# Kernel tuning notes

Hardware: AMD Instinct MI355X
Metric: run time of the kernel (lower is better)

The kernel has to match this reference:

```python
import jax, jax.numpy as jnp
import numpy as np
from jax import lax

BN_EPS = 1e-5
PAD = ((2, 3), (1, 2))  # 'same' padding for kernel (6,4): H pad 5 -> (2,3), W pad 3 -> (1,2)
DN = ('NCHW', 'OIHW', 'NCHW')


def _conv_block(x, w, b, g, bt, m, v, pool):
    # pool(bn(relu(conv(pad(x))))) as in the torch module (eval-mode BN)
    x = lax.conv_general_dilated(x, w, (1, 1), PAD, dimension_numbers=DN)
    x = jax.nn.relu(x + b[None, :, None, None])
    scale = g / jnp.sqrt(v + BN_EPS)
    x = (x - m[None, :, None, None]) * scale[None, :, None, None] + bt[None, :, None, None]
    win = (1, 1) + pool
    return lax.reduce_window(x, -jnp.inf, lax.max, win, win, 'VALID')


def _fc_bn(x, w, b, g, bt, m, v):
    x = jax.nn.relu(x @ w.T + b)
    return (x - m) * (g / jnp.sqrt(v + BN_EPS)) + bt


def _apply_cnn(x, p):
    x = x[:, None, :, :]  # [N,1,72,64]
    x = _conv_block(x, p['conv1_w'], p['conv1_b'], p['bnc1_g'], p['bnc1_b'], p['bnc1_m'], p['bnc1_v'], (2, 2))
    x = _conv_block(x, p['conv2_w'], p['conv2_b'], p['bnc2_g'], p['bnc2_b'], p['bnc2_m'], p['bnc2_v'], (2, 2))
    x = _conv_block(x, p['conv3_w'], p['conv3_b'], p['bnc3_g'], p['bnc3_b'], p['bnc3_m'], p['bnc3_v'], (3, 4))
    x = x.reshape(x.shape[0], 6 * 4 * 64)  # NCHW contiguous flatten matches torch .view
    x = _fc_bn(x, p['fc1_w'], p['fc1_b'], p['bnf1_g'], p['bnf1_b'], p['bnf1_m'], p['bnf1_v'])
    x = _fc_bn(x, p['fc2_w'], p['fc2_b'], p['bnf2_g'], p['bnf2_b'], p['bnf2_m'], p['bnf2_v'])
    x = _fc_bn(x, p['fc3_w'], p['fc3_b'], p['bnf3_g'], p['bnf3_b'], p['bnf3_m'], p['bnf3_v'])
    # F.normalize(x, p=2, dim=1) with eps=1e-12
    nrm = jnp.linalg.norm(x, axis=1, keepdims=True)
    return x / jnp.maximum(nrm, 1e-12)


def _ssm(embeds):
    # pairwise L2 distances via Gram trick (replaces the O(n^2) python loop)
    sq = jnp.sum(embeds * embeds, axis=1)  # [n]
    d2 = sq[:, None] + sq[None, :] - 2.0 * (embeds @ embeds.T)
    dist = jnp.sqrt(jnp.maximum(d2, 1e-12))
    dist = jnp.where(d2 > 0, dist, 0.0)  # exact zeros on diagonal, nan-safe grad
    return dist / jnp.max(dist)


def setup_inputs() -> dict:
    key = jax.random.key(0)
    ks = iter(jax.random.split(key, 64))
    d = {'x': jax.random.normal(next(ks), (512, 72, 64), jnp.float32)}

    def nrm(shape, s=0.05):
        return jax.random.normal(next(ks), shape, jnp.float32) * s

    def add_bn(name, c):
        d[name + '_g'] = 1.0 + nrm((c,))
        d[name + '_b'] = nrm((c,))
        d[name + '_m'] = nrm((c,), 0.1)
        d[name + '_v'] = 0.5 + jax.random.uniform(next(ks), (c,), jnp.float32)

    d['conv1_w'] = nrm((16, 1, 6, 4), 0.2);  d['conv1_b'] = nrm((16,));  add_bn('bnc1', 16)
    d['conv2_w'] = nrm((32, 16, 6, 4), 0.1); d['conv2_b'] = nrm((32,));  add_bn('bnc2', 32)
    d['conv3_w'] = nrm((64, 32, 6, 4), 0.05); d['conv3_b'] = nrm((64,)); add_bn('bnc3', 64)
    d['fc1_w'] = nrm((512, 1536), 0.03); d['fc1_b'] = nrm((512,)); add_bn('bnf1', 512)
    d['fc2_w'] = nrm((256, 512), 0.05);  d['fc2_b'] = nrm((256,)); add_bn('bnf2', 256)
    d['fc3_w'] = nrm((128, 256), 0.07);  d['fc3_b'] = nrm((128,)); add_bn('bnf3', 128)
    return d


def reference(x,
              conv1_w, conv1_b, bnc1_g, bnc1_b, bnc1_m, bnc1_v,
              conv2_w, conv2_b, bnc2_g, bnc2_b, bnc2_m, bnc2_v,
              conv3_w, conv3_b, bnc3_g, bnc3_b, bnc3_m, bnc3_v,
              fc1_w, fc1_b, bnf1_g, bnf1_b, bnf1_m, bnf1_v,
              fc2_w, fc2_b, bnf2_g, bnf2_b, bnf2_m, bnf2_v,
              fc3_w, fc3_b, bnf3_g, bnf3_b, bnf3_m, bnf3_v):
    p = dict(conv1_w=conv1_w, conv1_b=conv1_b, bnc1_g=bnc1_g, bnc1_b=bnc1_b, bnc1_m=bnc1_m, bnc1_v=bnc1_v,
             conv2_w=conv2_w, conv2_b=conv2_b, bnc2_g=bnc2_g, bnc2_b=bnc2_b, bnc2_m=bnc2_m, bnc2_v=bnc2_v,
             conv3_w=conv3_w, conv3_b=conv3_b, bnc3_g=bnc3_g, bnc3_b=bnc3_b, bnc3_m=bnc3_m, bnc3_v=bnc3_v,
             fc1_w=fc1_w, fc1_b=fc1_b, bnf1_g=bnf1_g, bnf1_b=bnf1_b, bnf1_m=bnf1_m, bnf1_v=bnf1_v,
             fc2_w=fc2_w, fc2_b=fc2_b, bnf2_g=bnf2_g, bnf2_b=bnf2_b, bnf2_m=bnf2_m, bnf2_v=bnf2_v,
             fc3_w=fc3_w, fc3_b=fc3_b, bnf3_g=bnf3_g, bnf3_b=bnf3_b, bnf3_m=bnf3_m, bnf3_v=bnf3_v)
    embeds = _apply_cnn(x, p)  # [n, 128], L2-normalized
    return _ssm(embeds)        # [n, n]
```

## Files before the change

kernel.cpp:

```cpp
#include <hip/hip_runtime.h>
#include <math.h>


#define BN_EPS 1e-5f

typedef __attribute__((ext_vector_type(8))) short short8;
typedef __attribute__((ext_vector_type(4))) float f32x4;

__device__ __forceinline__ unsigned short f2bf(float f) {
    unsigned u = __float_as_uint(f);
    u += 0x7fffu + ((u >> 16) & 1u);
    return (unsigned short)(u >> 16);
}

__global__ __launch_bounds__(256) void repack_k(
    const float* __restrict__ w1, const float* __restrict__ w2,
    const float* __restrict__ w3,
    const float* __restrict__ fw1, const float* __restrict__ fw2,
    const float* __restrict__ fw3,
    unsigned short* __restrict__ wT1b,
    unsigned short* __restrict__ wT2b, unsigned short* __restrict__ wT3b,
    unsigned short* __restrict__ fw1b, unsigned short* __restrict__ fw2b,
    unsigned short* __restrict__ fw3b, unsigned* __restrict__ mxslot)
{
    int t = blockIdx.x * 256 + threadIdx.x;
    if (t == 0) *mxslot = 0u;
    if (t < 512) {
        int k = t & 31, oc = t >> 5;
        wT1b[t] = (k < 24) ? f2bf(w1[oc * 24 + k]) : (unsigned short)0;
    }
    if (t < 12288) {
        int k = t & 31, oc = (t >> 5) & 31, kk = t >> 10;
        int ky = kk >> 1, kxp = kk & 1;
        int hi = k >> 4, ic = k & 15;
        int kx = 2 * kxp + hi;
        wT2b[t] = f2bf(w2[((oc * 16 + ic) * 6 + ky) * 4 + kx]);
    }
    if (t < 49152) {
        int ic = t & 31, oc = (t >> 5) & 63, kk = t >> 11;
        int ky = kk >> 2, kx = kk & 3;
        wT3b[t] = f2bf(w3[((oc * 32 + ic) * 6 + ky) * 4 + kx]);
    }
    if (t < 786432) fw1b[t] = f2bf(fw1[t]);
    if (t < 131072) fw2b[t] = f2bf(fw2[t]);
    if (t < 32768)  fw3b[t] = f2bf(fw3[t]);
}

__global__ __launch_bounds__(512) void conv_all(
    const float* __restrict__ x, const unsigned short* __restrict__ wT1,
    const unsigned short* __restrict__ wT2, const unsigned short* __restrict__ wT3,
    const float* __restrict__ c1b, const float* __restrict__ g1,
    const float* __restrict__ b1, const float* __restrict__ m1,
    const float* __restrict__ v1,
    const float* __restrict__ c2b, const float* __restrict__ g2,
    const float* __restrict__ b2, const float* __restrict__ m2,
    const float* __restrict__ v2,
    const float* __restrict__ c3b, const float* __restrict__ g3,
    const float* __restrict__ b3, const float* __restrict__ m3,
    const float* __restrict__ v3,
    unsigned short* __restrict__ out3)
{
    __shared__ __align__(16) unsigned short s_out1[2 * 1476 * 8];
    __shared__ __align__(16) unsigned short s_un[4 * 480 * 8];
    const int tid = threadIdx.x, nl = blockIdx.x;
    const int lane = tid & 63, wave = tid >> 6;
    const int n = lane & 15, q = lane >> 4;
    unsigned short* pa = s_un;
    unsigned short* pb = s_un + 5534;

    {
        unsigned* z32 = (unsigned*)s_un;
        for (int i = tid; i < 5532; i += 512) z32[i] = 0u;
        uint4 z4; z4.x = z4.y = z4.z = z4.w = 0u;
        for (int pc = tid; pc < 324; pc += 512) {
            int row, colc;
            if (pc < 180) { row = pc / 36; colc = pc % 36; if (row >= 2) row += 36; }
            else { int pz = pc - 180; row = 2 + (pz >> 2); colc = (pz & 3) ? 32 + (pz & 3) : 0; }
            int cc = row * 36 + colc;
            *(uint4*)(s_out1 + cc * 8) = z4;
            *(uint4*)(s_out1 + 11808 + cc * 8) = z4;
        }
    }
    __syncthreads();
    {
        const float4* src = (const float4*)(x + (size_t)nl * 4608);
        for (int i = tid; i < 1152; i += 512) {
            float4 val = src[i];
            int f = i * 4, row = (f >> 6) + 2, c = (f & 63) + 1;
            unsigned short h0 = f2bf(val.x), h1 = f2bf(val.y);
            unsigned short h2 = f2bf(val.z), h3 = f2bf(val.w);
            unsigned short* ap = pa + row * 70 + c;
            ap[0] = h0; ap[1] = h1; ap[2] = h2; ap[3] = h3;
            unsigned* bp = (unsigned*)(pb + row * 70 + c + 1);
            bp[0] = (unsigned)h0 | ((unsigned)h1 << 16);
            bp[1] = (unsigned)h2 | ((unsigned)h3 << 16);
        }
    }
    const float sc1 = g1[n] * rsqrtf(v1[n] + BN_EPS);
    const float bb1 = c1b[n];
    const float mm1 = b1[n] - m1[n] * sc1;
    const short8 bfr1 = *(const short8*)(wT1 + n * 32 + q * 8);
    __syncthreads();

    for (int i = 0; i < 36; ++i) {
        int t = wave * 36 + i;
        int pooled = 4 * t + (n >> 2);
        int ph = pooled >> 5, pw = pooled & 31;
        int py = (n >> 1) & 1, px = n & 1;
        int oh = 2 * ph + py, ow = 2 * pw + px;
        int r0 = (oh + 2 * q) * 70;
        const unsigned* base = px ? (const unsigned*)(pb + r0 + ow + 1)
                                  : (const unsigned*)(pa + r0 + ow);
        uint4 uu;
        uu.x = base[0];  uu.y = base[1];
        uu.z = base[35]; uu.w = base[36];
        short8 afr = *reinterpret_cast<short8*>(&uu);
        f32x4 acc = (f32x4){0.f, 0.f, 0.f, 0.f};
        acc = __builtin_amdgcn_mfma_f32_16x16x32_bf16(afr, bfr1, acc, 0, 0, 0);
        int po = 4 * t + q, oph = po >> 5, opw = po & 31;
        float mx = fmaxf(fmaxf(acc[0], acc[1]), fmaxf(acc[2], acc[3]));
        float val = fmaxf(mx + bb1, 0.f) * sc1 + mm1;
        int cc = (oph + 2) * 36 + (opw + 1);
        s_out1[(n >> 3) * 11808 + cc * 8 + (n & 7)] = f2bf(val);
    }
    __syncthreads();
    {
        uint4 z4; z4.x = z4.y = z4.z = z4.w = 0u;
        for (int pc = tid; pc < 192; pc += 512) {
            int row, colc;
            if (pc < 120) { row = pc / 20; colc = pc % 20; if (row >= 2) row += 18; }
            else { int pz = pc - 120; row = 2 + (pz >> 2); colc = (pz & 3) ? 16 + (pz & 3) : 0; }
            int cc = row * 20 + colc;
            *(uint4*)(s_un + cc * 8) = z4;
            *(uint4*)(s_un + 3840 + cc * 8) = z4;
            *(uint4*)(s_un + 7680 + cc * 8) = z4;
            *(uint4*)(s_un + 11520 + cc * 8) = z4;
        }
    }
    float bnb2[2], bns2[2], bnm2[2];
#pragma unroll
    for (int nt = 0; nt < 2; ++nt) {
        int oc = nt * 16 + n;
        float sc = g2[oc] * rsqrtf(v2[oc] + BN_EPS);
        bnb2[nt] = c2b[oc]; bns2[nt] = sc; bnm2[nt] = b2[oc] - m2[oc] * sc;
    }
    __syncthreads();

    for (int pp = wave; pp < 36; pp += 8) {
        int ph = pp >> 1, half = pp & 1;
        const unsigned short* bB = s_out1 + (q & 1) * 11808 + (q >> 1) * 8
                                   + (half * 16 + n) * 8 + (2 * ph) * 288;
        f32x4 acc[2][2];
#pragma unroll
        for (int ab = 0; ab < 2; ++ab)
#pragma unroll
            for (int nt = 0; nt < 2; ++nt) acc[ab][nt] = (f32x4){0.f, 0.f, 0.f, 0.f};
#pragma unroll
        for (int ky = 0; ky < 6; ++ky)
#pragma unroll
            for (int kxp = 0; kxp < 2; ++kxp) {
                int kk = ky * 2 + kxp;
                short8 w0 = *(const short8*)(wT2 + ((size_t)(kk * 32 + n) * 32) + q * 8);
                short8 w1 = *(const short8*)(wT2 + ((size_t)(kk * 32 + 16 + n) * 32) + q * 8);
#pragma unroll
                for (int ab = 0; ab < 2; ++ab) {
                    short8 afr = *(const short8*)(bB + ((ab + ky) * 288 + kxp * 16));
                    acc[ab][0] = __builtin_amdgcn_mfma_f32_16x16x32_bf16(afr, w0, acc[ab][0], 0, 0, 0);
                    acc[ab][1] = __builtin_amdgcn_mfma_f32_16x16x32_bf16(afr, w1, acc[ab][1], 0, 0, 0);
                }
            }
        int pw0 = half * 8 + q * 2;
#pragma unroll
        for (int nt = 0; nt < 2; ++nt) {
            int oc = nt * 16 + n;
            float p0 = fmaxf(fmaxf(acc[0][nt][0], acc[0][nt][1]),
                             fmaxf(acc[1][nt][0], acc[1][nt][1]));
            float p1 = fmaxf(fmaxf(acc[0][nt][2], acc[0][nt][3]),
                             fmaxf(acc[1][nt][2], acc[1][nt][3]));
            p0 = fmaxf(p0 + bnb2[nt], 0.f) * bns2[nt] + bnm2[nt];
            p1 = fmaxf(p1 + bnb2[nt], 0.f) * bns2[nt] + bnm2[nt];
            int cellA = (ph + 2) * 20 + pw0 + 1;
            int pl = (oc >> 3) * 3840, cl = oc & 7;
            s_un[pl + cellA * 8 + cl] = f2bf(p0);
            s_un[pl + (cellA + 1) * 8 + cl] = f2bf(p1);
        }
    }
    __syncthreads();

    for (int ch = wave; ch < 12; ch += 8) {
        int pr = ch >> 1, nth = ch & 1;
        const unsigned short* bC = s_un + q * 3840 + n * 8 + (3 * pr) * 160;
        f32x4 acc[3][2];
#pragma unroll
        for (int r = 0; r < 3; ++r)
#pragma unroll
            for (int t2 = 0; t2 < 2; ++t2) acc[r][t2] = (f32x4){0.f, 0.f, 0.f, 0.f};
#pragma unroll
        for (int ky = 0; ky < 6; ++ky)
#pragma unroll
            for (int kx = 0; kx < 4; ++kx) {
                int kk = ky * 4 + kx;
                short8 w0 = *(const short8*)(wT3 + ((size_t)(kk * 64 + nth * 32 + n) * 32) + q * 8);
                short8 w1 = *(const short8*)(wT3 + ((size_t)(kk * 64 + nth * 32 + 16 + n) * 32) + q * 8);
#pragma unroll
                for (int r = 0; r < 3; ++r) {
                    short8 afr = *(const short8*)(bC + ((r + ky) * 160 + kx * 8));
                    acc[r][0] = __builtin_amdgcn_mfma_f32_16x16x32_bf16(afr, w0, acc[r][0], 0, 0, 0);
                    acc[r][1] = __builtin_amdgcn_mfma_f32_16x16x32_bf16(afr, w1, acc[r][1], 0, 0, 0);
                }
            }
        size_t ob = (size_t)nl * 1536;
#pragma unroll
        for (int t2 = 0; t2 < 2; ++t2) {
            int oc = nth * 32 + t2 * 16 + n;
            float sc = g3[oc] * rsqrtf(v3[oc] + BN_EPS);
            float mx = -3.4e38f;
#pragma unroll
            for (int r = 0; r < 3; ++r)
#pragma unroll
                for (int e = 0; e < 4; ++e) mx = fmaxf(mx, acc[r][t2][e]);
            float val = fmaxf(mx + c3b[oc], 0.f) * sc + (b3[oc] - m3[oc] * sc);
            out3[ob + (size_t)oc * 24 + pr * 4 + q] = f2bf(val);
        }
    }
}

__global__ __launch_bounds__(256) void fc_m(
    const unsigned short* __restrict__ A, const unsigned short* __restrict__ W,
    const float* __restrict__ bias, const float* __restrict__ g,
    const float* __restrict__ bt, const float* __restrict__ m,
    const float* __restrict__ v, unsigned short* __restrict__ out_b,
    float* __restrict__ out_f, int K, int N, int mode)
{
    const int tid = threadIdx.x;
    const int lane = tid & 63, wave = tid >> 6;
    const int n = lane & 15, q = lane >> 4;
    const int wr = wave >> 1, wc = wave & 1;
    const int r0 = blockIdx.y * 32 + wr * 16;
    const int c0 = blockIdx.x * 32 + wc * 16;
    const int col = c0 + n;

    float sc = g[col] * rsqrtf(v[col] + BN_EPS);
    float bb = bias[col];
    float mm = bt[col] - m[col] * sc;

    const unsigned short* Ap = A + (size_t)(r0 + n) * K + q * 8;
    const unsigned short* Bp = W + (size_t)col * K + q * 8;

    f32x4 acc0 = (f32x4){0.f, 0.f, 0.f, 0.f};
    f32x4 acc1 = (f32x4){0.f, 0.f, 0.f, 0.f};
    short8 a0 = *(const short8*)(Ap);
    short8 b0 = *(const short8*)(Bp);
    short8 a1 = *(const short8*)(Ap + 32);
    short8 b1 = *(const short8*)(Bp + 32);
#pragma unroll 2
    for (int kk = 64; kk < K; kk += 64) {
        short8 a0n = *(const short8*)(Ap + kk);
        short8 b0n = *(const short8*)(Bp + kk);
        short8 a1n = *(const short8*)(Ap + kk + 32);
        short8 b1n = *(const short8*)(Bp + kk + 32);
        acc0 = __builtin_amdgcn_mfma_f32_16x16x32_bf16(a0, b0, acc0, 0, 0, 0);
        acc1 = __builtin_amdgcn_mfma_f32_16x16x32_bf16(a1, b1, acc1, 0, 0, 0);
        a0 = a0n; b0 = b0n; a1 = a1n; b1 = b1n;
    }
    acc0 = __builtin_amdgcn_mfma_f32_16x16x32_bf16(a0, b0, acc0, 0, 0, 0);
    acc1 = __builtin_amdgcn_mfma_f32_16x16x32_bf16(a1, b1, acc1, 0, 0, 0);
#pragma unroll
    for (int e = 0; e < 4; ++e) {
        int row = r0 + q * 4 + e;
        float val = fmaxf(acc0[e] + acc1[e] + bb, 0.f) * sc + mm;
        if (mode == 0) out_b[(size_t)row * N + col] = f2bf(val);
        else           out_f[(size_t)row * N + col] = val;
    }
}

__global__ __launch_bounds__(128) void norm_k(const float* __restrict__ f3,
                                              float* __restrict__ E,
                                              float* __restrict__ sq)
{
    __shared__ float red[2];
    const int row = blockIdx.x, tid = threadIdx.x;
    float vv = f3[row * 128 + tid];
    float s = vv * vv;
#pragma unroll
    for (int off = 32; off >= 1; off >>= 1) s += __shfl_down(s, off, 64);
    if ((tid & 63) == 0) red[tid >> 6] = s;
    __syncthreads();
    float total = red[0] + red[1];
    float nn = fmaxf(sqrtf(total), 1e-12f);
    E[row * 128 + tid] = vv / nn;
    if (tid == 0) sq[row] = total / (nn * nn);
}

__global__ __launch_bounds__(256) void dist_k(const float* __restrict__ E,
                                              const float* __restrict__ sq,
                                              float* __restrict__ D,
                                              unsigned* __restrict__ mxslot)
{
    __shared__ __align__(16) float Ei[16 * 132];
    __shared__ __align__(16) float Ej[16 * 132];
    __shared__ float red[256];
    const int tid = threadIdx.x;
    const int bi = blockIdx.y * 16, bj = blockIdx.x * 16;
    {
        int lr = tid >> 4, lc = (tid & 15) * 8;
        float4 a0 = *(const float4*)(E + (bi + lr) * 128 + lc);
        float4 a1 = *(const float4*)(E + (bi + lr) * 128 + lc + 4);
        *(float4*)(Ei + lr * 132 + lc) = a0;
        *(float4*)(Ei + lr * 132 + lc + 4) = a1;
        float4 b0 = *(const float4*)(E + (bj + lr) * 128 + lc);
        float4 b1 = *(const float4*)(E + (bj + lr) * 128 + lc + 4);
        *(float4*)(Ej + lr * 132 + lc) = b0;
        *(float4*)(Ej + lr * 132 + lc + 4) = b1;
    }
    __syncthreads();
    const int tx = tid & 15, ty = tid >> 4;
    float dot = 0.f;
#pragma unroll 4
    for (int k = 0; k < 128; k += 4) {
        float4 a = *(const float4*)(Ei + ty * 132 + k);
        float4 b = *(const float4*)(Ej + tx * 132 + k);
        dot = fmaf(a.x, b.x, dot); dot = fmaf(a.y, b.y, dot);
        dot = fmaf(a.z, b.z, dot); dot = fmaf(a.w, b.w, dot);
    }
    int i = bi + ty, j = bj + tx;
    float d2 = sq[i] + sq[j] - 2.f * dot;
    float dist = sqrtf(fmaxf(d2, 1e-12f));
    dist = (d2 > 0.f) ? dist : 0.f;
    if (i == j) dist = 0.f;
    D[i * 512 + j] = dist;
    red[tid] = dist;
    __syncthreads();
    for (int s2 = 128; s2 > 0; s2 >>= 1) {
        if (tid < s2) red[tid] = fmaxf(red[tid], red[tid + s2]);
        __syncthreads();
    }
    if (tid == 0) atomicMax(mxslot, __float_as_uint(red[0]));
}

__global__ __launch_bounds__(256) void scale_k(float* __restrict__ D,
                                               const unsigned* __restrict__ mxslot)
{
    int idx = blockIdx.x * 256 + threadIdx.x;
    float M = __uint_as_float(*mxslot);
    D[idx] = D[idx] / M;
}

extern "C" void kernel_launch(void* const* d_in, const int* in_sizes, int n_in,
                              void* d_out, int out_size, void* d_ws, size_t ws_size,
                              hipStream_t stream)
{
    (void)in_sizes; (void)n_in; (void)out_size; (void)ws_size;
    const float* x    = (const float*)d_in[0];
    const float* c1w  = (const float*)d_in[1];
    const float* c1b  = (const float*)d_in[2];
    const float* g1   = (const float*)d_in[3];
    const float* b1   = (const float*)d_in[4];
    const float* m1   = (const float*)d_in[5];
    const float* v1   = (const float*)d_in[6];
    const float* c2w  = (const float*)d_in[7];
    const float* c2b  = (const float*)d_in[8];
    const float* g2   = (const float*)d_in[9];
    const float* b2   = (const float*)d_in[10];
    const float* m2   = (const float*)d_in[11];
    const float* v2   = (const float*)d_in[12];
    const float* c3w  = (const float*)d_in[13];
    const float* c3b  = (const float*)d_in[14];
    const float* g3   = (const float*)d_in[15];
    const float* b3   = (const float*)d_in[16];
    const float* m3   = (const float*)d_in[17];
    const float* v3   = (const float*)d_in[18];
    const float* fw1  = (const float*)d_in[19];
    const float* fb1  = (const float*)d_in[20];
    const float* gf1  = (const float*)d_in[21];
    const float* bf1  = (const float*)d_in[22];
    const float* mf1  = (const float*)d_in[23];
    const float* vf1  = (const float*)d_in[24];
    const float* fw2  = (const float*)d_in[25];
    const float* fb2  = (const float*)d_in[26];
    const float* gf2  = (const float*)d_in[27];
    const float* bf2  = (const float*)d_in[28];
    const float* mf2  = (const float*)d_in[29];
    const float* vf2  = (const float*)d_in[30];
    const float* fw3  = (const float*)d_in[31];
    const float* fb3  = (const float*)d_in[32];
    const float* gf3  = (const float*)d_in[33];
    const float* bf3  = (const float*)d_in[34];
    const float* mf3  = (const float*)d_in[35];
    const float* vf3  = (const float*)d_in[36];

    float* ws = (float*)d_ws;
    float* E    = ws + 0;
    float* sq   = ws + 65536;
    float* f3v  = ws + 66048;
    unsigned* mx = (unsigned*)(ws + 131584);
    unsigned short* wT1b = (unsigned short*)(ws + 131600);
    unsigned short* wT2b = (unsigned short*)(ws + 131856);
    unsigned short* wT3b = (unsigned short*)(ws + 138000);
    unsigned short* fw1b = (unsigned short*)(ws + 162576);
    unsigned short* fw2b = (unsigned short*)(ws + 555792);
    unsigned short* fw3b = (unsigned short*)(ws + 621328);
    unsigned short* out3b= (unsigned short*)(ws + 637712);
    unsigned short* a1b  = (unsigned short*)(ws + 1030928);
    unsigned short* a2b  = (unsigned short*)(ws + 1162000);

    float* out = (float*)d_out;

    repack_k<<<3072, 256, 0, stream>>>(c1w, c2w, c3w, fw1, fw2, fw3,
                                       wT1b, wT2b, wT3b, fw1b, fw2b, fw3b, mx);
    conv_all<<<512, 512, 0, stream>>>(x, wT1b, wT2b, wT3b,
                                      c1b, g1, b1, m1, v1,
                                      c2b, g2, b2, m2, v2,
                                      c3b, g3, b3, m3, v3, out3b);
    fc_m<<<dim3(16, 16), 256, 0, stream>>>(out3b, fw1b, fb1, gf1, bf1, mf1, vf1,
                                           a1b, nullptr, 1536, 512, 0);
    fc_m<<<dim3(8, 16), 256, 0, stream>>>(a1b, fw2b, fb2, gf2, bf2, mf2, vf2,
                                          a2b, nullptr, 512, 256, 0);
    fc_m<<<dim3(4, 16), 256, 0, stream>>>(a2b, fw3b, fb3, gf3, bf3, mf3, vf3,
                                          nullptr, f3v, 256, 128, 1);
    norm_k<<<512, 128, 0, stream>>>(f3v, E, sq);
    dist_k<<<dim3(32, 32), 256, 0, stream>>>(E, sq, out, mx);
    scale_k<<<1024, 256, 0, stream>>>(out, mx);
}
```

Measured before the change: 217.6 us.

## Convert FC weights in-kernel and fuse norm, distance and scaling with grid barrier

The FC weight bf16 conversion moves out of the repack kernel and into the fc_m inner loop, which now reads fp32 weights and converts them per load. The norm, dist and scale kernels merge into one kernel. Each block normalizes its own rows, computes distances, then waits at a software grid-wide barrier (atomic counter and spin) for the global max before dividing. This removes two launches and the intermediate round trips of the E and D buffers. In exchange, fc weights are read as fp32 (twice the bytes) and converted by every block that uses them. The spin barrier also relies on all 1024 blocks being resident at once.

```diff
diff --git a/kernel.cpp b/kernel.cpp
--- a/kernel.cpp
+++ b/kernel.cpp
@@ -13,18 +13,24 @@
     return (unsigned short)(u >> 16);
 }
 
+__device__ __forceinline__ short8 f2bf8(float4 lo, float4 hi) {
+    short8 r;
+    r[0] = (short)f2bf(lo.x); r[1] = (short)f2bf(lo.y);
+    r[2] = (short)f2bf(lo.z); r[3] = (short)f2bf(lo.w);
+    r[4] = (short)f2bf(hi.x); r[5] = (short)f2bf(hi.y);
+    r[6] = (short)f2bf(hi.z); r[7] = (short)f2bf(hi.w);
+    return r;
+}
+
 __global__ __launch_bounds__(256) void repack_k(
     const float* __restrict__ w1, const float* __restrict__ w2,
     const float* __restrict__ w3,
-    const float* __restrict__ fw1, const float* __restrict__ fw2,
-    const float* __restrict__ fw3,
     unsigned short* __restrict__ wT1b,
     unsigned short* __restrict__ wT2b, unsigned short* __restrict__ wT3b,
-    unsigned short* __restrict__ fw1b, unsigned short* __restrict__ fw2b,
-    unsigned short* __restrict__ fw3b, unsigned* __restrict__ mxslot)
+    unsigned* __restrict__ mxslot, unsigned* __restrict__ done)
 {
     int t = blockIdx.x * 256 + threadIdx.x;
-    if (t == 0) *mxslot = 0u;
+    if (t == 0) { *mxslot = 0u; *done = 0u; }
     if (t < 512) {
         int k = t & 31, oc = t >> 5;
         wT1b[t] = (k < 24) ? f2bf(w1[oc * 24 + k]) : (unsigned short)0;
@@ -41,9 +47,6 @@
         int ky = kk >> 2, kx = kk & 3;
         wT3b[t] = f2bf(w3[((oc * 32 + ic) * 6 + ky) * 4 + kx]);
     }
-    if (t < 786432) fw1b[t] = f2bf(fw1[t]);
-    if (t < 131072) fw2b[t] = f2bf(fw2[t]);
-    if (t < 32768)  fw3b[t] = f2bf(fw3[t]);
 }
 
 __global__ __launch_bounds__(512) void conv_all(
@@ -226,7 +229,7 @@
 }
 
 __global__ __launch_bounds__(256) void fc_m(
-    const unsigned short* __restrict__ A, const unsigned short* __restrict__ W,
+    const unsigned short* __restrict__ A, const float* __restrict__ W,
     const float* __restrict__ bias, const float* __restrict__ g,
     const float* __restrict__ bt, const float* __restrict__ m,
     const float* __restrict__ v, unsigned short* __restrict__ out_b,
@@ -245,23 +248,26 @@
     float mm = bt[col] - m[col] * sc;
 
     const unsigned short* Ap = A + (size_t)(r0 + n) * K + q * 8;
-    const unsigned short* Bp = W + (size_t)col * K + q * 8;
+    const float* Bp = W + (size_t)col * K + q * 8;
 
     f32x4 acc0 = (f32x4){0.f, 0.f, 0.f, 0.f};
     f32x4 acc1 = (f32x4){0.f, 0.f, 0.f, 0.f};
     short8 a0 = *(const short8*)(Ap);
-    short8 b0 = *(const short8*)(Bp);
     short8 a1 = *(const short8*)(Ap + 32);
-    short8 b1 = *(const short8*)(Bp + 32);
+    short8 b0 = f2bf8(*(const float4*)(Bp), *(const float4*)(Bp + 4));
+    short8 b1 = f2bf8(*(const float4*)(Bp + 32), *(const float4*)(Bp + 36));
 #pragma unroll 2
     for (int kk = 64; kk < K; kk += 64) {
         short8 a0n = *(const short8*)(Ap + kk);
-        short8 b0n = *(const short8*)(Bp + kk);
         short8 a1n = *(const short8*)(Ap + kk + 32);
-        short8 b1n = *(const short8*)(Bp + kk + 32);
+        float4 c0a = *(const float4*)(Bp + kk);
+        float4 c0b = *(const float4*)(Bp + kk + 4);
+        float4 c1a = *(const float4*)(Bp + kk + 32);
+        float4 c1b = *(const float4*)(Bp + kk + 36);
         acc0 = __builtin_amdgcn_mfma_f32_16x16x32_bf16(a0, b0, acc0, 0, 0, 0);
         acc1 = __builtin_amdgcn_mfma_f32_16x16x32_bf16(a1, b1, acc1, 0, 0, 0);
-        a0 = a0n; b0 = b0n; a1 = a1n; b1 = b1n;
+        a0 = a0n; a1 = a1n;
+        b0 = f2bf8(c0a, c0b); b1 = f2bf8(c1a, c1b);
     }
     acc0 = __builtin_amdgcn_mfma_f32_16x16x32_bf16(a0, b0, acc0, 0, 0, 0);
     acc1 = __builtin_amdgcn_mfma_f32_16x16x32_bf16(a1, b1, acc1, 0, 0, 0);
@@ -274,44 +280,45 @@
     }
 }
 
-__global__ __launch_bounds__(128) void norm_k(const float* __restrict__ f3,
-                                              float* __restrict__ E,
-                                              float* __restrict__ sq)
-{
-    __shared__ float red[2];
-    const int row = blockIdx.x, tid = threadIdx.x;
-    float vv = f3[row * 128 + tid];
-    float s = vv * vv;
-#pragma unroll
-    for (int off = 32; off >= 1; off >>= 1) s += __shfl_down(s, off, 64);
-    if ((tid & 63) == 0) red[tid >> 6] = s;
-    __syncthreads();
-    float total = red[0] + red[1];
-    float nn = fmaxf(sqrtf(total), 1e-12f);
-    E[row * 128 + tid] = vv / nn;
-    if (tid == 0) sq[row] = total / (nn * nn);
-}
-
-__global__ __launch_bounds__(256) void dist_k(const float* __restrict__ E,
-                                              const float* __restrict__ sq,
-                                              float* __restrict__ D,
-                                              unsigned* __restrict__ mxslot)
+__global__ __launch_bounds__(256, 4) void normdist_k(
+    const float* __restrict__ f3, float* __restrict__ D,
+    unsigned* __restrict__ mxslot, unsigned* __restrict__ done)
 {
     __shared__ __align__(16) float Ei[16 * 132];
     __shared__ __align__(16) float Ej[16 * 132];
+    __shared__ float sqi[16], sqj[16];
     __shared__ float red[256];
     const int tid = threadIdx.x;
     const int bi = blockIdx.y * 16, bj = blockIdx.x * 16;
     {
         int lr = tid >> 4, lc = (tid & 15) * 8;
-        float4 a0 = *(const float4*)(E + (bi + lr) * 128 + lc);
-        float4 a1 = *(const float4*)(E + (bi + lr) * 128 + lc + 4);
+        float4 a0 = *(const float4*)(f3 + (bi + lr) * 128 + lc);
+        float4 a1 = *(const float4*)(f3 + (bi + lr) * 128 + lc + 4);
+        float4 b0 = *(const float4*)(f3 + (bj + lr) * 128 + lc);
+        float4 b1 = *(const float4*)(f3 + (bj + lr) * 128 + lc + 4);
+        float sa = a0.x*a0.x + a0.y*a0.y + a0.z*a0.z + a0.w*a0.w
+                 + a1.x*a1.x + a1.y*a1.y + a1.z*a1.z + a1.w*a1.w;
+        float sb = b0.x*b0.x + b0.y*b0.y + b0.z*b0.z + b0.w*b0.w
+                 + b1.x*b1.x + b1.y*b1.y + b1.z*b1.z + b1.w*b1.w;
+#pragma unroll
+        for (int mk = 1; mk <= 8; mk <<= 1) {
+            sa += __shfl_xor(sa, mk, 64);
+            sb += __shfl_xor(sb, mk, 64);
+        }
+        float nna = fmaxf(sqrtf(sa), 1e-12f);
+        float nnb = fmaxf(sqrtf(sb), 1e-12f);
+        a0.x /= nna; a0.y /= nna; a0.z /= nna; a0.w /= nna;
+        a1.x /= nna; a1.y /= nna; a1.z /= nna; a1.w /= nna;
+        b0.x /= nnb; b0.y /= nnb; b0.z /= nnb; b0.w /= nnb;
+        b1.x /= nnb; b1.y /= nnb; b1.z /= nnb; b1.w /= nnb;
         *(float4*)(Ei + lr * 132 + lc) = a0;
         *(float4*)(Ei + lr * 132 + lc + 4) = a1;
-        float4 b0 = *(const float4*)(E + (bj + lr) * 128 + lc);
-        float4 b1 = *(const float4*)(E + (bj + lr) * 128 + lc + 4);
         *(float4*)(Ej + lr * 132 + lc) = b0;
         *(float4*)(Ej + lr * 132 + lc + 4) = b1;
+        if ((tid & 15) == 0) {
+            sqi[lr] = sa / (nna * nna);
+            sqj[lr] = sb / (nnb * nnb);
+        }
     }
     __syncthreads();
     const int tx = tid & 15, ty = tid >> 4;
@@ -324,26 +331,27 @@
         dot = fmaf(a.z, b.z, dot); dot = fmaf(a.w, b.w, dot);
     }
     int i = bi + ty, j = bj + tx;
-    float d2 = sq[i] + sq[j] - 2.f * dot;
+    float d2 = sqi[ty] + sqj[tx] - 2.f * dot;
     float dist = sqrtf(fmaxf(d2, 1e-12f));
     dist = (d2 > 0.f) ? dist : 0.f;
     if (i == j) dist = 0.f;
-    D[i * 512 + j] = dist;
     red[tid] = dist;
     __syncthreads();
     for (int s2 = 128; s2 > 0; s2 >>= 1) {
         if (tid < s2) red[tid] = fmaxf(red[tid], red[tid + s2]);
         __syncthreads();
     }
-    if (tid == 0) atomicMax(mxslot, __float_as_uint(red[0]));
-}
-
-__global__ __launch_bounds__(256) void scale_k(float* __restrict__ D,
-                                               const unsigned* __restrict__ mxslot)
-{
-    int idx = blockIdx.x * 256 + threadIdx.x;
-    float M = __uint_as_float(*mxslot);
-    D[idx] = D[idx] / M;
+    if (tid == 0) {
+        atomicMax(mxslot, __float_as_uint(red[0]));
+        __threadfence();
+        atomicAdd(done, 1u);
+        unsigned vv;
+        do { __builtin_amdgcn_s_sleep(2); vv = atomicMax(done, 0u); }
+        while (vv < 1024u);
+        red[0] = __uint_as_float(atomicMax(mxslot, 0u));
+    }
+    __syncthreads();
+    D[i * 512 + j] = dist / red[0];
 }
 
 extern "C" void kernel_launch(void* const* d_in, const int* in_sizes, int n_in,
@@ -390,35 +398,28 @@
     const float* vf3  = (const float*)d_in[36];
 
     float* ws = (float*)d_ws;
-    float* E    = ws + 0;
-    float* sq   = ws + 65536;
     float* f3v  = ws + 66048;
-    unsigned* mx = (unsigned*)(ws + 131584);
+    unsigned* mx   = (unsigned*)(ws + 131584);
+    unsigned* done = (unsigned*)(ws + 131585);
     unsigned short* wT1b = (unsigned short*)(ws + 131600);
     unsigned short* wT2b = (unsigned short*)(ws + 131856);
     unsigned short* wT3b = (unsigned short*)(ws + 138000);
-    unsigned short* fw1b = (unsigned short*)(ws + 162576);
-    unsigned short* fw2b = (unsigned short*)(ws + 555792);
-    unsigned short* fw3b = (unsigned short*)(ws + 621328);
     unsigned short* out3b= (unsigned short*)(ws + 637712);
     unsigned short* a1b  = (unsigned short*)(ws + 1030928);
     unsigned short* a2b  = (unsigned short*)(ws + 1162000);
 
     float* out = (float*)d_out;
 
-    repack_k<<<3072, 256, 0, stream>>>(c1w, c2w, c3w, fw1, fw2, fw3,
-                                       wT1b, wT2b, wT3b, fw1b, fw2b, fw3b, mx);
+    repack_k<<<192, 256, 0, stream>>>(c1w, c2w, c3w, wT1b, wT2b, wT3b, mx, done);
     conv_all<<<512, 512, 0, stream>>>(x, wT1b, wT2b, wT3b,
                                       c1b, g1, b1, m1, v1,
                                       c2b, g2, b2, m2, v2,
                                       c3b, g3, b3, m3, v3, out3b);
-    fc_m<<<dim3(16, 16), 256, 0, stream>>>(out3b, fw1b, fb1, gf1, bf1, mf1, vf1,
+    fc_m<<<dim3(16, 16), 256, 0, stream>>>(out3b, fw1, fb1, gf1, bf1, mf1, vf1,
                                            a1b, nullptr, 1536, 512, 0);
-    fc_m<<<dim3(8, 16), 256, 0, stream>>>(a1b, fw2b, fb2, gf2, bf2, mf2, vf2,
+    fc_m<<<dim3(8, 16), 256, 0, stream>>>(a1b, fw2, fb2, gf2, bf2, mf2, vf2,
                                           a2b, nullptr, 512, 256, 0);
-    fc_m<<<dim3(4, 16), 256, 0, stream>>>(a2b, fw3b, fb3, gf3, bf3, mf3, vf3,
+    fc_m<<<dim3(4, 16), 256, 0, stream>>>(a2b, fw3, fb3, gf3, bf3, mf3, vf3,
                                           nullptr, f3v, 256, 128, 1);
-    norm_k<<<512, 128, 0, stream>>>(f3v, E, sq);
-    dist_k<<<dim3(32, 32), 256, 0, stream>>>(E, sq, out, mx);
-    scale_k<<<1024, 256, 0, stream>>>(out, mx);
-}
+    normdist_k<<<dim3(32, 32), 256, 0, stream>>>(f3v, out, mx, done);
+}
```

Measured after the change: 282.0 us. 1.3x slower.
